# Performance work log

Hardware: AMD Instinct MI355X
Metric: run time of the kernel (lower is better)

Reference implementation:

```python
import jax, jax.numpy as jnp
import numpy as np

D_IN, D_OUT, HEADS, D_K = 256, 256, 8, 32
B, N, L = 2, 128, 512
SCALING = 1.0 / np.sqrt(D_K)


def setup_inputs() -> dict:
    key = jax.random.key(0)
    ks = jax.random.split(key, 12)
    s = 0.02
    return {
        "query": jax.random.normal(ks[0], (B, L, D_IN), jnp.float32),
        "key": jax.random.normal(ks[1], (B, L, D_IN), jnp.float32),
        "value": jax.random.normal(ks[2], (B, N, L, D_OUT), jnp.float32),
        "mask": jax.random.uniform(ks[3], (B, 1, L, L), jnp.float32),
        "Wq": jax.random.normal(ks[4], (D_IN, HEADS * D_K), jnp.float32) * s,
        "bq": jnp.zeros((HEADS * D_K,), jnp.float32),
        "Wk": jax.random.normal(ks[5], (D_IN, HEADS * D_K), jnp.float32) * s,
        "bk": jnp.zeros((HEADS * D_K,), jnp.float32),
        "Wv": jax.random.normal(ks[6], (D_OUT, D_OUT), jnp.float32) * s,
        "bv": jnp.zeros((D_OUT,), jnp.float32),
        "Wo": jax.random.normal(ks[7], (D_OUT, D_OUT), jnp.float32) * s,
        "bo": jnp.zeros((D_OUT,), jnp.float32),
    }


def reference(query, key, value, mask, Wq, bq, Wk, bk, Wv, bv, Wo, bo):
    b, n, l = value.shape[:3]
    h, dk = HEADS, D_K
    dh = value.shape[-1] // h  # per-head value dim
    # projections -> per-head layouts
    q = (query @ Wq + bq).reshape(b, l, h, dk).transpose(0, 2, 1, 3)  # bhld
    k = (key @ Wk + bk).reshape(b, l, h, dk).transpose(0, 2, 1, 3)    # bhld
    v = (value @ Wv + bv).reshape(b, n, l, h, dh).transpose(0, 3, 1, 2, 4)  # bhnld
    q = q * SCALING
    scores = jnp.einsum('bhid,bhjd->bhij', q, k)  # (B,H,L,L)
    scores = jnp.where(mask < 0.5, jnp.finfo(scores.dtype).min, scores)
    attn = jax.nn.softmax(scores, axis=-1)
    # dropout omitted (eval mode / deterministic reference)
    out = jnp.einsum('bhij,bhnjd->bhnid', attn, v)  # (B,H,N,L,dh)
    out = out.transpose(0, 2, 3, 1, 4).reshape(b, n, l, h * dh)
    return out @ Wo + bo
```

## Files before the change

### kernel.cpp

```cpp
#include <hip/hip_runtime.h>
#include <hip/hip_bf16.h>
#include <stdint.h>

#define BB 2
#define LL 512
#define DIN 256
#define HH 8
#define DKK 32
#define NN 128
#define DM 256
#define SCALING 0.17677669529663687f

typedef unsigned short u16;
typedef float f32x4 __attribute__((ext_vector_type(4)));
typedef short s16x8 __attribute__((ext_vector_type(8)));

#define MFMA16(a, b, c) __builtin_amdgcn_mfma_f32_16x16x32_bf16((a), (b), (c), 0, 0, 0)

typedef __attribute__((address_space(3))) char lds_char;
typedef const __attribute__((address_space(1))) char glb_char;

__device__ __forceinline__ void gload16(const void* g, void* l) {
    __builtin_amdgcn_global_load_lds((glb_char*)g, (lds_char*)l, 16, 0, 0);
}

__device__ __forceinline__ u16 f2bf(float f) {
    union { float f; uint32_t i; } v; v.f = f;
    uint32_t x = v.i;
    return (u16)((x + 0x7fffu + ((x >> 16) & 1u)) >> 16);
}

__device__ __forceinline__ uint32_t pack2bf(float f0, float f1) {
    union { float f; uint32_t i; } a, b;
    a.f = f0; b.f = f1;
    return __builtin_amdgcn_perm(b.i + 0x8000u, a.i + 0x8000u, 0x07060302u);
}

__device__ __forceinline__ s16x8 ldsfrag(const u16* base, int row, int cb) {
    const char* p = (const char*)base + row * 128 + (cb ^ ((row & 7) << 4));
    return *(const s16x8*)(const void*)p;
}

__global__ __launch_bounds__(256) void prep_weights(
        const float* __restrict__ Wq, const float* __restrict__ Wk,
        const float* __restrict__ Wv, const float* __restrict__ Wo,
        u16* __restrict__ wqt, u16* __restrict__ wkt,
        u16* __restrict__ wvt, u16* __restrict__ wot) {
    int idx = blockIdx.x * 256 + threadIdx.x;
    int which = idx >> 16;
    const float* src = (which == 0) ? Wq : (which == 1) ? Wk : (which == 2) ? Wv : Wo;
    u16* dst = (which == 0) ? wqt : (which == 1) ? wkt : (which == 2) ? wvt : wot;
    int i = idx & 65535;
    int c = i & 255;
    int k = i >> 8;
    dst[(size_t)c * 256 + k] = f2bf(src[(size_t)k * 256 + c]);
}

__global__ __launch_bounds__(256) void qk_proj(
        const float* __restrict__ q_in, const float* __restrict__ k_in,
        const u16* __restrict__ wqt, const float* __restrict__ bq,
        const u16* __restrict__ wkt, const float* __restrict__ bk,
        u16* __restrict__ q_ws, u16* __restrict__ k_ws) {
    int bid = blockIdx.x;
    int isK = bid & 1;
    int r0 = (bid >> 1) * 64;
    const float* src = isK ? k_in : q_in;
    const u16* wt    = isK ? wkt : wqt;
    const float* bias = isK ? bk : bq;
    u16* dst = isK ? k_ws : q_ws;
    float scale = isK ? 1.0f : SCALING;

    int t = threadIdx.x, w = t >> 6, l = t & 63, lr = l & 15, lg = l >> 4;

    f32x4 zero = {0.f, 0.f, 0.f, 0.f};
    f32x4 acc[4][4];
#pragma unroll
    for (int m = 0; m < 4; m++)
#pragma unroll
        for (int cf = 0; cf < 4; cf++) acc[m][cf] = zero;

#pragma unroll
    for (int ks = 0; ks < 8; ks++) {
        s16x8 afr[4];
#pragma unroll
        for (int m = 0; m < 4; m++) {
            const float* p = src + (size_t)(r0 + m * 16 + lr) * DIN + ks * 32 + lg * 8;
            float4 v0 = *(const float4*)p;
            float4 v1 = *(const float4*)(p + 4);
            union { u16 u[8]; s16x8 v; } tmp;
            tmp.u[0] = f2bf(v0.x); tmp.u[1] = f2bf(v0.y);
            tmp.u[2] = f2bf(v0.z); tmp.u[3] = f2bf(v0.w);
            tmp.u[4] = f2bf(v1.x); tmp.u[5] = f2bf(v1.y);
            tmp.u[6] = f2bf(v1.z); tmp.u[7] = f2bf(v1.w);
            afr[m] = tmp.v;
        }
        s16x8 bfrg[4];
#pragma unroll
        for (int cf = 0; cf < 4; cf++)
            bfrg[cf] = *(const s16x8*)(const void*)(wt + (size_t)(w * 64 + cf * 16 + lr) * 256 + ks * 32 + lg * 8);
#pragma unroll
        for (int m = 0; m < 4; m++)
#pragma unroll
            for (int cf = 0; cf < 4; cf++) acc[m][cf] = MFMA16(afr[m], bfrg[cf], acc[m][cf]);
    }

#pragma unroll
    for (int m = 0; m < 4; m++)
#pragma unroll
        for (int cf = 0; cf < 4; cf++) {
            int c = w * 64 + cf * 16 + lr;
            int h = c >> 5, dd = c & 31;
            float bv_ = bias[c];
#pragma unroll
            for (int r = 0; r < 4; r++) {
                int row = r0 + m * 16 + 4 * lg + r;
                int b = row >> 9, li = row & 511;
                dst[(((size_t)(b * HH + h)) * LL + li) * DKK + dd] = f2bf((acc[m][cf][r] + bv_) * scale);
            }
        }
}

__global__ __launch_bounds__(256) void scores_softmax(
        const u16* __restrict__ q_ws, const u16* __restrict__ k_ws,
        const float* __restrict__ mask, u16* __restrict__ attn) {
    int bid = blockIdx.x;
    int it = bid & 15;
    int bh = bid >> 4;
    int b = bh >> 3;
    int i0 = it * 32;

    __shared__ u16 kl[LL][40];
    __shared__ u16 ql[32][40];
    __shared__ float redmx[2][32];
    __shared__ float redsm[2][32];

    int t = threadIdx.x;
    const u16* kbase = k_ws + (size_t)bh * LL * DKK;
#pragma unroll
    for (int x = 0; x < 8; x++) {
        int idx = x * 256 + t;
        int row = idx >> 2, ch = idx & 3;
        *(s16x8*)(void*)(&kl[row][ch * 8]) = *(const s16x8*)(const void*)(kbase + (size_t)row * DKK + ch * 8);
    }
    if (t < 128) {
        const u16* qbase = q_ws + (size_t)bh * LL * DKK + (size_t)i0 * DKK;
        int row = t >> 2, ch = t & 3;
        *(s16x8*)(void*)(&ql[row][ch * 8]) = *(const s16x8*)(const void*)(qbase + (size_t)row * DKK + ch * 8);
    }
    __syncthreads();

    int w = t >> 6, l = t & 63, lr = l & 15, lg = l >> 4;
    int ih = (w & 1) * 16;
    int jh = (w >> 1) * 256;
    int jhalf = w >> 1;

    s16x8 af = *(const s16x8*)(const void*)(&ql[ih + lr][lg * 8]);
    f32x4 zero = {0.f, 0.f, 0.f, 0.f};
    f32x4 acc[16];
#pragma unroll
    for (int cf = 0; cf < 16; cf++) {
        s16x8 bf = *(const s16x8*)(const void*)(&kl[jh + cf * 16 + lr][lg * 8]);
        acc[cf] = MFMA16(af, bf, zero);
    }

    const float* mrow = mask + (size_t)b * LL * LL;
    float attv[16][4];
    float mx[4], sm[4];
#pragma unroll
    for (int r = 0; r < 4; r++) mx[r] = -3.0e38f;
#pragma unroll
    for (int cf = 0; cf < 16; cf++) {
#pragma unroll
        for (int r = 0; r < 4; r++) {
            int irow = i0 + ih + 4 * lg + r;
            int jcol = jh + cf * 16 + lr;
            float mv = mrow[(size_t)irow * LL + jcol];
            float s = (mv < 0.5f) ? -1.0e30f : acc[cf][r];
            attv[cf][r] = s;
            mx[r] = fmaxf(mx[r], s);
        }
    }
#pragma unroll
    for (int d = 1; d < 16; d <<= 1)
#pragma unroll
        for (int r = 0; r < 4; r++) mx[r] = fmaxf(mx[r], __shfl_xor(mx[r], d));
#pragma unroll
    for (int r = 0; r < 4; r++) sm[r] = 0.f;
#pragma unroll
    for (int cf = 0; cf < 16; cf++)
#pragma unroll
        for (int r = 0; r < 4; r++) {
            float p = __expf(attv[cf][r] - mx[r]);
            attv[cf][r] = p;
            sm[r] += p;
        }
#pragma unroll
    for (int d = 1; d < 16; d <<= 1)
#pragma unroll
        for (int r = 0; r < 4; r++) sm[r] += __shfl_xor(sm[r], d);

    if (lr == 0) {
#pragma unroll
        for (int r = 0; r < 4; r++) {
            redmx[jhalf][ih + 4 * lg + r] = mx[r];
            redsm[jhalf][ih + 4 * lg + r] = sm[r];
        }
    }
    __syncthreads();
    float inv[4];
#pragma unroll
    for (int r = 0; r < 4; r++) {
        int row = ih + 4 * lg + r;
        float m0 = redmx[0][row], m1 = redmx[1][row];
        float s0 = redsm[0][row], s1 = redsm[1][row];
        float gm = fmaxf(m0, m1);
        float gs = s0 * __expf(m0 - gm) + s1 * __expf(m1 - gm);
        inv[r] = __expf(mx[r] - gm) / gs;
    }

    u16* abase = attn + (size_t)bh * LL * LL;
#pragma unroll
    for (int cf = 0; cf < 16; cf++)
#pragma unroll
        for (int r = 0; r < 4; r++) {
            int irow = i0 + ih + 4 * lg + r;
            int jcol = jh + cf * 16 + lr;
            abase[(size_t)irow * LL + jcol] = f2bf(attv[cf][r] * inv[r]);
        }
}

__global__ __launch_bounds__(256, 2) void vproj_gemm(
        const float* __restrict__ value, const float* __restrict__ bv,
        const u16* __restrict__ wvt, u16* __restrict__ ut) {
    __shared__ __align__(16) u16 sm[2 * 16384];

    int t = threadIdx.x;
    int nb = gridDim.x;
    int cpx = nb >> 3;
    int swz = (blockIdx.x & 7) * cpx + (blockIdx.x >> 3);
    int ct = swz & 1;
    int jt = (swz >> 1) & 3;
    int bn = swz >> 3;
    int c0 = ct * 128, j0 = jt * 128;

    int w = t >> 6, l = t & 63, lr = l & 15, lg = l >> 4;
    int wr = w >> 1, wc = w & 1;

    const float* vbase = value + ((size_t)bn * LL + j0) * DM;

    int srow = t >> 3;
    int sgc = t & 7;
    f32x4 zero = {0.f, 0.f, 0.f, 0.f};
    f32x4 acc[4][4];
#pragma unroll
    for (int m = 0; m < 4; m++)
#pragma unroll
        for (int nf = 0; nf < 4; nf++) acc[m][nf] = zero;

    auto stageA = [&](int buf, int kk) {
#pragma unroll
        for (int x = 0; x < 4; x++) {
            int row = x * 32 + srow;
            int gs = sgc ^ (row & 7);
            gload16(wvt + (size_t)(c0 + row) * 256 + kk * 64 + gs * 8,
                    (char*)&sm[buf * 16384] + (x * 256 + t) * 16);
        }
    };
    float4 breg[2][4][2];
    auto loadB = [&](int set, int kk) {
#pragma unroll
        for (int x = 0; x < 4; x++) {
            int row = x * 32 + srow;
            const float* p = vbase + (size_t)row * DM + kk * 64 + sgc * 8;
            breg[set][x][0] = *(const float4*)p;
            breg[set][x][1] = *(const float4*)(p + 4);
        }
    };
    auto writeB = [&](int buf, int set) {
#pragma unroll
        for (int x = 0; x < 4; x++) {
            int row = x * 32 + srow;
            uint32_t p0 = pack2bf(breg[set][x][0].x, breg[set][x][0].y);
            uint32_t p1 = pack2bf(breg[set][x][0].z, breg[set][x][0].w);
            uint32_t p2 = pack2bf(breg[set][x][1].x, breg[set][x][1].y);
            uint32_t p3 = pack2bf(breg[set][x][1].z, breg[set][x][1].w);
            uint32_t* dst = (uint32_t*)((char*)&sm[buf * 16384 + 8192]
                            + row * 128 + ((sgc * 16) ^ ((row & 7) << 4)));
            dst[0] = p0; dst[1] = p1; dst[2] = p2; dst[3] = p3;
        }
    };

    stageA(0, 0);
    loadB(0, 0);
    loadB(1, 1);
    writeB(0, 0);
    __syncthreads();
    int cur = 0;
#pragma unroll
    for (int kk = 0; kk < 4; kk++) {
        if (kk < 3) stageA(cur ^ 1, kk + 1);
        if (kk < 2) loadB(kk & 1, kk + 2);
        const u16* Ab = &sm[cur * 16384];
        const u16* Bb = &sm[cur * 16384 + 8192];
        s16x8 af[4][2], bf[4][2];
#pragma unroll
        for (int m = 0; m < 4; m++)
#pragma unroll
            for (int ks = 0; ks < 2; ks++)
                af[m][ks] = ldsfrag(Ab, wr * 64 + m * 16 + lr, ks * 64 + lg * 16);
#pragma unroll
        for (int nf = 0; nf < 4; nf++)
#pragma unroll
            for (int ks = 0; ks < 2; ks++)
                bf[nf][ks] = ldsfrag(Bb, wc * 64 + nf * 16 + lr, ks * 64 + lg * 16);
#pragma unroll
        for (int ks = 0; ks < 2; ks++)
#pragma unroll
            for (int m = 0; m < 4; m++)
#pragma unroll
                for (int nf = 0; nf < 4; nf++)
                    acc[m][nf] = MFMA16(af[m][ks], bf[nf][ks], acc[m][nf]);
        if (kk < 3) writeB(cur ^ 1, (kk + 1) & 1);
        __syncthreads();
        cur ^= 1;
    }

    u16* ubase = ut + (size_t)bn * DM * LL;
#pragma unroll
    for (int m = 0; m < 4; m++) {
#pragma unroll
        for (int rr = 0; rr < 4; rr++) {
            int c = c0 + wr * 64 + m * 16 + 4 * lg + rr;
            float bvv = bv[c];
#pragma unroll
            for (int nf = 0; nf < 4; nf++) {
                int j = j0 + wc * 64 + nf * 16 + lr;
                ubase[(size_t)c * LL + j] = f2bf(acc[m][nf][rr] + bvv);
            }
        }
    }
}

__global__ __launch_bounds__(256, 2) void pv_gemm(
        const u16* __restrict__ attn, const u16* __restrict__ ut,
        u16* __restrict__ Tm, int n0, int nTiles, int Nc) {
    __shared__ __align__(16) u16 sm[2 * 16384];

    int t = threadIdx.x;
    int nb = gridDim.x;
    int cpx = nb >> 3;
    int swz = (blockIdx.x & 7) * cpx + (blockIdx.x >> 3);
    int nct = swz % nTiles;
    int tmp2 = swz / nTiles;
    int it = tmp2 & 3;
    int bh = tmp2 >> 2;
    int b = bh >> 3, h = bh & 7;
    int i0 = it * 128;

    int w = t >> 6, l = t & 63, lr = l & 15, lg = l >> 4;
    int wr = w >> 1, wc = w & 1;

    const u16* arow0 = attn + (size_t)bh * LL * LL + (size_t)i0 * LL;

    f32x4 zero = {0.f, 0.f, 0.f, 0.f};
    f32x4 acc[4][4];
#pragma unroll
    for (int m = 0; m < 4; m++)
#pragma unroll
        for (int nf = 0; nf < 4; nf++) acc[m][nf] = zero;

    auto stage = [&](int buf, int kk) {
#pragma unroll
        for (int x = 0; x < 4; x++) {
            int G = x * 256 + t;
            int row = G >> 3, gc = G & 7;
            int gs = gc ^ (row & 7);
            gload16(arow0 + (size_t)row * LL + kk * 64 + gs * 8,
                    (char*)&sm[buf * 16384] + G * 16);
        }
#pragma unroll
        for (int x = 0; x < 4; x++) {
            int G = x * 256 + t;
            int row = G >> 3, gc = G & 7;
            int gs = gc ^ (row & 7);
            int nc = nct * 128 + row;
            const u16* src = ut + (((size_t)(b * NN + n0 + (nc >> 5))) * DM + h * DKK + (nc & 31)) * LL
                             + kk * 64 + gs * 8;
            gload16(src, (char*)&sm[buf * 16384 + 8192] + G * 16);
        }
    };

    stage(0, 0);
    __syncthreads();
    int cur = 0;
    for (int kk = 0; kk < 8; kk++) {
        if (kk < 7) stage(cur ^ 1, kk + 1);
        const u16* Ab = &sm[cur * 16384];
        const u16* Bb = &sm[cur * 16384 + 8192];
        s16x8 af[4][2], bf[4][2];
#pragma unroll
        for (int m = 0; m < 4; m++)
#pragma unroll
            for (int ks = 0; ks < 2; ks++)
                af[m][ks] = ldsfrag(Ab, wr * 64 + m * 16 + lr, ks * 64 + lg * 16);
#pragma unroll
        for (int nf = 0; nf < 4; nf++)
#pragma unroll
            for (int ks = 0; ks < 2; ks++)
                bf[nf][ks] = ldsfrag(Bb, wc * 64 + nf * 16 + lr, ks * 64 + lg * 16);
#pragma unroll
        for (int ks = 0; ks < 2; ks++)
#pragma unroll
            for (int m = 0; m < 4; m++)
#pragma unroll
                for (int nf = 0; nf < 4; nf++)
                    acc[m][nf] = MFMA16(af[m][ks], bf[nf][ks], acc[m][nf]);
        __syncthreads();
        cur ^= 1;
    }

#pragma unroll
    for (int m = 0; m < 4; m++) {
        int i = i0 + wr * 64 + m * 16 + 4 * lg;
#pragma unroll
        for (int nf = 0; nf < 4; nf++) {
            int nc = nct * 128 + wc * 64 + nf * 16 + lr;
            int nl = nc >> 5, cl = nc & 31;
            u16* dst = Tm + (((size_t)(b * Nc + nl)) * LL + i) * DM + h * DKK + cl;
#pragma unroll
            for (int rr = 0; rr < 4; rr++)
                dst[(size_t)rr * DM] = f2bf(acc[m][nf][rr]);
        }
    }
}

__global__ __launch_bounds__(256, 2) void wo_gemm(
        const u16* __restrict__ Tm, const u16* __restrict__ wot,
        const float* __restrict__ bo, float* __restrict__ out,
        int n0, int Nc, int nshift) {
    __shared__ __align__(16) u16 sm[2 * 16384];

    int t = threadIdx.x;
    int nb = gridDim.x;
    int cpx = nb >> 3;
    int swz = (blockIdx.x & 7) * cpx + (blockIdx.x >> 3);
    int oc = swz & 1;
    int mt = swz >> 1;
    int r0 = mt * 128;

    int w = t >> 6, l = t & 63, lr = l & 15, lg = l >> 4;
    int wr = w >> 1, wc = w & 1;

    f32x4 zero = {0.f, 0.f, 0.f, 0.f};
    f32x4 acc[4][4];
#pragma unroll
    for (int m = 0; m < 4; m++)
#pragma unroll
        for (int nf = 0; nf < 4; nf++) acc[m][nf] = zero;

    auto stage = [&](int buf, int kk) {
#pragma unroll
        for (int x = 0; x < 4; x++) {
            int G = x * 256 + t;
            int row = G >> 3, gc = G & 7;
            int gs = gc ^ (row & 7);
            gload16(Tm + (size_t)(r0 + row) * DM + kk * 64 + gs * 8,
                    (char*)&sm[buf * 16384] + G * 16);
        }
#pragma unroll
        for (int x = 0; x < 4; x++) {
            int G = x * 256 + t;
            int row = G >> 3, gc = G & 7;
            int gs = gc ^ (row & 7);
            gload16(wot + (size_t)(oc * 128 + row) * DM + kk * 64 + gs * 8,
                    (char*)&sm[buf * 16384 + 8192] + G * 16);
        }
    };

    stage(0, 0);
    __syncthreads();
    int cur = 0;
    for (int kk = 0; kk < 4; kk++) {
        if (kk < 3) stage(cur ^ 1, kk + 1);
        const u16* Ab = &sm[cur * 16384];
        const u16* Bb = &sm[cur * 16384 + 8192];
        s16x8 af[4][2], bf[4][2];
#pragma unroll
        for (int m = 0; m < 4; m++)
#pragma unroll
            for (int ks = 0; ks < 2; ks++)
                af[m][ks] = ldsfrag(Ab, wr * 64 + m * 16 + lr, ks * 64 + lg * 16);
#pragma unroll
        for (int nf = 0; nf < 4; nf++)
#pragma unroll
            for (int ks = 0; ks < 2; ks++)
                bf[nf][ks] = ldsfrag(Bb, wc * 64 + nf * 16 + lr, ks * 64 + lg * 16);
#pragma unroll
        for (int ks = 0; ks < 2; ks++)
#pragma unroll
            for (int m = 0; m < 4; m++)
#pragma unroll
                for (int nf = 0; nf < 4; nf++)
                    acc[m][nf] = MFMA16(af[m][ks], bf[nf][ks], acc[m][nf]);
        __syncthreads();
        cur ^= 1;
    }

#pragma unroll
    for (int nf = 0; nf < 4; nf++) {
        int ocol = oc * 128 + wc * 64 + nf * 16 + lr;
        float bov = bo[ocol];
#pragma unroll
        for (int m = 0; m < 4; m++) {
            int rbase = r0 + wr * 64 + m * 16 + 4 * lg;
#pragma unroll
            for (int rr = 0; rr < 4; rr++) {
                int r = rbase + rr;
                int bnl = r >> 9, i = r & 511;
                int b = bnl >> nshift, nl = bnl & (Nc - 1);
                out[(((size_t)(b * NN + n0 + nl)) * LL + i) * DM + ocol] = acc[m][nf][rr] + bov;
            }
        }
    }
}

extern "C" void kernel_launch(void* const* d_in, const int* in_sizes, int n_in,
                              void* d_out, int out_size, void* d_ws, size_t ws_size,
                              hipStream_t stream) {
    const float* query = (const float*)d_in[0];
    const float* key_  = (const float*)d_in[1];
    const float* value = (const float*)d_in[2];
    const float* mask  = (const float*)d_in[3];
    const float* Wq = (const float*)d_in[4];
    const float* bq = (const float*)d_in[5];
    const float* Wk = (const float*)d_in[6];
    const float* bk = (const float*)d_in[7];
    const float* Wv = (const float*)d_in[8];
    const float* bv = (const float*)d_in[9];
    const float* Wo = (const float*)d_in[10];
    const float* bo = (const float*)d_in[11];

    char* ws = (char*)d_ws;
    u16* wvt  = (u16*)(ws + 0);
    u16* wot  = (u16*)(ws + 131072);
    u16* qw   = (u16*)(ws + 262144);
    u16* kw   = (u16*)(ws + 786432);
    u16* attn = (u16*)(ws + 1310720);
    u16* wqt  = (u16*)(ws + 1310720);
    u16* wkt  = (u16*)(ws + 1310720 + 131072);
    u16* ut   = (u16*)(ws + 9699328);
    u16* Tm   = (u16*)(ws + 76808192);
    float* out = (float*)d_out;

    size_t avail = (ws_size > 76808192u) ? (ws_size - 76808192u) : 0;
    int Nc = 128;
    while (Nc > 4 && (size_t)Nc * 524288u > avail) Nc >>= 1;
    int nshift = 0;
    while ((1 << nshift) < Nc) nshift++;

    hipLaunchKernelGGL(prep_weights,   dim3(1024), dim3(256), 0, stream, Wq, Wk, Wv, Wo, wqt, wkt, wvt, wot);
    hipLaunchKernelGGL(qk_proj,        dim3(32),   dim3(256), 0, stream, query, key_, wqt, bq, wkt, bk, qw, kw);
    hipLaunchKernelGGL(scores_softmax, dim3(256),  dim3(256), 0, stream, qw, kw, mask, attn);
    hipLaunchKernelGGL(vproj_gemm,     dim3(2048), dim3(256), 0, stream, value, bv, wvt, ut);

    int nTiles = Nc >> 2;
    for (int n0 = 0; n0 < NN; n0 += Nc) {
        hipLaunchKernelGGL(pv_gemm, dim3(16 * 4 * nTiles), dim3(256), 0, stream,
                           attn, ut, Tm, n0, nTiles, Nc);
        hipLaunchKernelGGL(wo_gemm, dim3((BB * Nc * LL / 128) * 2), dim3(256), 0, stream,
                           Tm, wot, bo, out, n0, Nc, nshift);
    }
}
```

Before: 185.0 us.

## Deepen pv_gemm pipeline to four stages with BK=32 and vmcnt waits

Reworks the PV GEMM main loop from a double-buffered BK=64 pipeline into a four-buffer BK=32 ring with three stages of loads in flight. It uses explicit s_waitcnt vmcnt counts and a single barrier per iteration instead of waiting on all loads and syncing twice. The goal is to hide global-to-LDS load latency behind MFMA work. LDS size stays the same, but there are twice as many iterations and barriers, and the swizzle for the 64-byte rows now only spreads over 4 positions, which may cause more bank conflicts.

```diff
diff --git a/kernel.cpp b/kernel.cpp
--- a/kernel.cpp
+++ b/kernel.cpp
@@ -38,6 +38,11 @@
 
 __device__ __forceinline__ s16x8 ldsfrag(const u16* base, int row, int cb) {
     const char* p = (const char*)base + row * 128 + (cb ^ ((row & 7) << 4));
+    return *(const s16x8*)(const void*)p;
+}
+
+__device__ __forceinline__ s16x8 ldsfrag32(const u16* base, int row, int lg) {
+    const char* p = (const char*)base + row * 64 + ((lg * 16) ^ ((row & 3) << 4));
     return *(const s16x8*)(const void*)p;
 }
 
@@ -344,7 +349,7 @@
 __global__ __launch_bounds__(256, 2) void pv_gemm(
         const u16* __restrict__ attn, const u16* __restrict__ ut,
         u16* __restrict__ Tm, int n0, int nTiles, int Nc) {
-    __shared__ __align__(16) u16 sm[2 * 16384];
+    __shared__ __align__(16) u16 sm[4 * 8192];
 
     int t = threadIdx.x;
     int nb = gridDim.x;
@@ -371,52 +376,49 @@
 
     auto stage = [&](int buf, int kk) {
 #pragma unroll
-        for (int x = 0; x < 4; x++) {
+        for (int x = 0; x < 2; x++) {
             int G = x * 256 + t;
-            int row = G >> 3, gc = G & 7;
-            int gs = gc ^ (row & 7);
-            gload16(arow0 + (size_t)row * LL + kk * 64 + gs * 8,
-                    (char*)&sm[buf * 16384] + G * 16);
-        }
-#pragma unroll
-        for (int x = 0; x < 4; x++) {
+            int row = G >> 2, gc = G & 3;
+            int gs = gc ^ (row & 3);
+            gload16(arow0 + (size_t)row * LL + kk * 32 + gs * 8,
+                    (char*)&sm[buf * 8192] + G * 16);
+        }
+#pragma unroll
+        for (int x = 0; x < 2; x++) {
             int G = x * 256 + t;
-            int row = G >> 3, gc = G & 7;
-            int gs = gc ^ (row & 7);
+            int row = G >> 2, gc = G & 3;
+            int gs = gc ^ (row & 3);
             int nc = nct * 128 + row;
             const u16* src = ut + (((size_t)(b * NN + n0 + (nc >> 5))) * DM + h * DKK + (nc & 31)) * LL
-                             + kk * 64 + gs * 8;
-            gload16(src, (char*)&sm[buf * 16384 + 8192] + G * 16);
+                             + kk * 32 + gs * 8;
+            gload16(src, (char*)&sm[buf * 8192 + 4096] + G * 16);
         }
     };
 
     stage(0, 0);
-    __syncthreads();
-    int cur = 0;
-    for (int kk = 0; kk < 8; kk++) {
-        if (kk < 7) stage(cur ^ 1, kk + 1);
-        const u16* Ab = &sm[cur * 16384];
-        const u16* Bb = &sm[cur * 16384 + 8192];
-        s16x8 af[4][2], bf[4][2];
+    stage(1, 1);
+    stage(2, 2);
+#pragma unroll
+    for (int kk = 0; kk < 16; kk++) {
+        if (kk <= 13)      asm volatile("s_waitcnt vmcnt(8)" ::: "memory");
+        else if (kk == 14) asm volatile("s_waitcnt vmcnt(4)" ::: "memory");
+        else               asm volatile("s_waitcnt vmcnt(0)" ::: "memory");
+        __builtin_amdgcn_s_barrier();
+        if (kk < 13) stage((kk + 3) & 3, kk + 3);
+        const u16* Ab = &sm[(kk & 3) * 8192];
+        const u16* Bb = &sm[(kk & 3) * 8192 + 4096];
+        s16x8 af[4], bf[4];
 #pragma unroll
         for (int m = 0; m < 4; m++)
-#pragma unroll
-            for (int ks = 0; ks < 2; ks++)
-                af[m][ks] = ldsfrag(Ab, wr * 64 + m * 16 + lr, ks * 64 + lg * 16);
+            af[m] = ldsfrag32(Ab, wr * 64 + m * 16 + lr, lg);
 #pragma unroll
         for (int nf = 0; nf < 4; nf++)
-#pragma unroll
-            for (int ks = 0; ks < 2; ks++)
-                bf[nf][ks] = ldsfrag(Bb, wc * 64 + nf * 16 + lr, ks * 64 + lg * 16);
-#pragma unroll
-        for (int ks = 0; ks < 2; ks++)
-#pragma unroll
-            for (int m = 0; m < 4; m++)
-#pragma unroll
-                for (int nf = 0; nf < 4; nf++)
-                    acc[m][nf] = MFMA16(af[m][ks], bf[nf][ks], acc[m][nf]);
-        __syncthreads();
-        cur ^= 1;
+            bf[nf] = ldsfrag32(Bb, wc * 64 + nf * 16 + lr, lg);
+#pragma unroll
+        for (int m = 0; m < 4; m++)
+#pragma unroll
+            for (int nf = 0; nf < 4; nf++)
+                acc[m][nf] = MFMA16(af[m], bf[nf], acc[m][nf]);
     }
 
 #pragma unroll
```

Result: slower. 192.6 us (+4.1%).

## Fuse scores-softmax and V projection into one heterogeneous launch

Applied to the files above, without the earlier changes.

Merges the independent scores/softmax kernel and the V-projection GEMM into a single grid, where block index selects which task to run. This removes one launch and lets the small softmax work overlap with the large GEMM instead of running serially. The fused kernel loses the explicit launch bounds and the softmax blocks now reserve the larger shared buffer, which may change register allocation and occupancy.

```diff
diff --git a/kernel.cpp b/kernel.cpp
--- a/kernel.cpp
+++ b/kernel.cpp
@@ -120,224 +120,223 @@
         }
 }
 
-__global__ __launch_bounds__(256) void scores_softmax(
+__global__ void sv_fused(
+        const float* __restrict__ value, const float* __restrict__ bv,
+        const u16* __restrict__ wvt, u16* __restrict__ ut,
         const u16* __restrict__ q_ws, const u16* __restrict__ k_ws,
         const float* __restrict__ mask, u16* __restrict__ attn) {
-    int bid = blockIdx.x;
-    int it = bid & 15;
-    int bh = bid >> 4;
-    int b = bh >> 3;
-    int i0 = it * 32;
-
-    __shared__ u16 kl[LL][40];
-    __shared__ u16 ql[32][40];
-    __shared__ float redmx[2][32];
-    __shared__ float redsm[2][32];
+    __shared__ __align__(16) u16 sm[2 * 16384];
 
     int t = threadIdx.x;
-    const u16* kbase = k_ws + (size_t)bh * LL * DKK;
-#pragma unroll
-    for (int x = 0; x < 8; x++) {
-        int idx = x * 256 + t;
-        int row = idx >> 2, ch = idx & 3;
-        *(s16x8*)(void*)(&kl[row][ch * 8]) = *(const s16x8*)(const void*)(kbase + (size_t)row * DKK + ch * 8);
-    }
-    if (t < 128) {
-        const u16* qbase = q_ws + (size_t)bh * LL * DKK + (size_t)i0 * DKK;
-        int row = t >> 2, ch = t & 3;
-        *(s16x8*)(void*)(&ql[row][ch * 8]) = *(const s16x8*)(const void*)(qbase + (size_t)row * DKK + ch * 8);
-    }
-    __syncthreads();
-
     int w = t >> 6, l = t & 63, lr = l & 15, lg = l >> 4;
-    int ih = (w & 1) * 16;
-    int jh = (w >> 1) * 256;
-    int jhalf = w >> 1;
-
-    s16x8 af = *(const s16x8*)(const void*)(&ql[ih + lr][lg * 8]);
-    f32x4 zero = {0.f, 0.f, 0.f, 0.f};
-    f32x4 acc[16];
-#pragma unroll
-    for (int cf = 0; cf < 16; cf++) {
-        s16x8 bf = *(const s16x8*)(const void*)(&kl[jh + cf * 16 + lr][lg * 8]);
-        acc[cf] = MFMA16(af, bf, zero);
-    }
-
-    const float* mrow = mask + (size_t)b * LL * LL;
-    float attv[16][4];
-    float mx[4], sm[4];
-#pragma unroll
-    for (int r = 0; r < 4; r++) mx[r] = -3.0e38f;
-#pragma unroll
-    for (int cf = 0; cf < 16; cf++) {
+
+    if (blockIdx.x < 2048) {
+        int bid = blockIdx.x;
+        int cpx = 2048 >> 3;
+        int swz = (bid & 7) * cpx + (bid >> 3);
+        int ct = swz & 1;
+        int jt = (swz >> 1) & 3;
+        int bn = swz >> 3;
+        int c0 = ct * 128, j0 = jt * 128;
+        int wr = w >> 1, wc = w & 1;
+
+        const float* vbase = value + ((size_t)bn * LL + j0) * DM;
+        int srow = t >> 3;
+        int sgc = t & 7;
+        f32x4 zero = {0.f, 0.f, 0.f, 0.f};
+        f32x4 acc[4][4];
+#pragma unroll
+        for (int m = 0; m < 4; m++)
+#pragma unroll
+            for (int nf = 0; nf < 4; nf++) acc[m][nf] = zero;
+
+        auto stageA = [&](int buf, int kk) {
+#pragma unroll
+            for (int x = 0; x < 4; x++) {
+                int row = x * 32 + srow;
+                int gs = sgc ^ (row & 7);
+                gload16(wvt + (size_t)(c0 + row) * 256 + kk * 64 + gs * 8,
+                        (char*)&sm[buf * 16384] + (x * 256 + t) * 16);
+            }
+        };
+        float4 breg[2][4][2];
+        auto loadB = [&](int set, int kk) {
+#pragma unroll
+            for (int x = 0; x < 4; x++) {
+                int row = x * 32 + srow;
+                const float* p = vbase + (size_t)row * DM + kk * 64 + sgc * 8;
+                breg[set][x][0] = *(const float4*)p;
+                breg[set][x][1] = *(const float4*)(p + 4);
+            }
+        };
+        auto writeB = [&](int buf, int set) {
+#pragma unroll
+            for (int x = 0; x < 4; x++) {
+                int row = x * 32 + srow;
+                uint32_t p0 = pack2bf(breg[set][x][0].x, breg[set][x][0].y);
+                uint32_t p1 = pack2bf(breg[set][x][0].z, breg[set][x][0].w);
+                uint32_t p2 = pack2bf(breg[set][x][1].x, breg[set][x][1].y);
+                uint32_t p3 = pack2bf(breg[set][x][1].z, breg[set][x][1].w);
+                uint32_t* dst = (uint32_t*)((char*)&sm[buf * 16384 + 8192]
+                                + row * 128 + ((sgc * 16) ^ ((row & 7) << 4)));
+                dst[0] = p0; dst[1] = p1; dst[2] = p2; dst[3] = p3;
+            }
+        };
+
+        stageA(0, 0);
+        loadB(0, 0);
+        loadB(1, 1);
+        writeB(0, 0);
+        __syncthreads();
+        int cur = 0;
+#pragma unroll
+        for (int kk = 0; kk < 4; kk++) {
+            if (kk < 3) stageA(cur ^ 1, kk + 1);
+            if (kk < 2) loadB(kk & 1, kk + 2);
+            const u16* Ab = &sm[cur * 16384];
+            const u16* Bb = &sm[cur * 16384 + 8192];
+            s16x8 af[4][2], bf[4][2];
+#pragma unroll
+            for (int m = 0; m < 4; m++)
+#pragma unroll
+                for (int ks = 0; ks < 2; ks++)
+                    af[m][ks] = ldsfrag(Ab, wr * 64 + m * 16 + lr, ks * 64 + lg * 16);
+#pragma unroll
+            for (int nf = 0; nf < 4; nf++)
+#pragma unroll
+                for (int ks = 0; ks < 2; ks++)
+                    bf[nf][ks] = ldsfrag(Bb, wc * 64 + nf * 16 + lr, ks * 64 + lg * 16);
+#pragma unroll
+            for (int ks = 0; ks < 2; ks++)
+#pragma unroll
+                for (int m = 0; m < 4; m++)
+#pragma unroll
+                    for (int nf = 0; nf < 4; nf++)
+                        acc[m][nf] = MFMA16(af[m][ks], bf[nf][ks], acc[m][nf]);
+            if (kk < 3) writeB(cur ^ 1, (kk + 1) & 1);
+            __syncthreads();
+            cur ^= 1;
+        }
+
+        u16* ubase = ut + (size_t)bn * DM * LL;
+#pragma unroll
+        for (int m = 0; m < 4; m++) {
+#pragma unroll
+            for (int rr = 0; rr < 4; rr++) {
+                int c = c0 + wr * 64 + m * 16 + 4 * lg + rr;
+                float bvv = bv[c];
+#pragma unroll
+                for (int nf = 0; nf < 4; nf++) {
+                    int j = j0 + wc * 64 + nf * 16 + lr;
+                    ubase[(size_t)c * LL + j] = f2bf(acc[m][nf][rr] + bvv);
+                }
+            }
+        }
+    } else {
+        int bid = blockIdx.x - 2048;
+        int it = bid & 15;
+        int bh = bid >> 4;
+        int b = bh >> 3;
+        int i0 = it * 32;
+
+        u16* kl_ = sm;
+        u16* ql_ = sm + 20480;
+        float* redmx_ = (float*)(void*)(sm + 21760);
+        float* redsm_ = redmx_ + 64;
+
+        const u16* kbase = k_ws + (size_t)bh * LL * DKK;
+#pragma unroll
+        for (int x = 0; x < 8; x++) {
+            int idx = x * 256 + t;
+            int row = idx >> 2, ch = idx & 3;
+            *(s16x8*)(void*)(kl_ + row * 40 + ch * 8) =
+                *(const s16x8*)(const void*)(kbase + (size_t)row * DKK + ch * 8);
+        }
+        if (t < 128) {
+            const u16* qbase = q_ws + (size_t)bh * LL * DKK + (size_t)i0 * DKK;
+            int row = t >> 2, ch = t & 3;
+            *(s16x8*)(void*)(ql_ + row * 40 + ch * 8) =
+                *(const s16x8*)(const void*)(qbase + (size_t)row * DKK + ch * 8);
+        }
+        __syncthreads();
+
+        int ih = (w & 1) * 16;
+        int jh = (w >> 1) * 256;
+        int jhalf = w >> 1;
+
+        s16x8 af = *(const s16x8*)(const void*)(ql_ + (ih + lr) * 40 + lg * 8);
+        f32x4 zero = {0.f, 0.f, 0.f, 0.f};
+        f32x4 acc[16];
+#pragma unroll
+        for (int cf = 0; cf < 16; cf++) {
+            s16x8 bf = *(const s16x8*)(const void*)(kl_ + (jh + cf * 16 + lr) * 40 + lg * 8);
+            acc[cf] = MFMA16(af, bf, zero);
+        }
+
+        const float* mrow = mask + (size_t)b * LL * LL;
+        float attv[16][4];
+        float mx[4], smax[4];
+#pragma unroll
+        for (int r = 0; r < 4; r++) mx[r] = -3.0e38f;
+#pragma unroll
+        for (int cf = 0; cf < 16; cf++) {
+#pragma unroll
+            for (int r = 0; r < 4; r++) {
+                int irow = i0 + ih + 4 * lg + r;
+                int jcol = jh + cf * 16 + lr;
+                float mv = mrow[(size_t)irow * LL + jcol];
+                float s = (mv < 0.5f) ? -1.0e30f : acc[cf][r];
+                attv[cf][r] = s;
+                mx[r] = fmaxf(mx[r], s);
+            }
+        }
+#pragma unroll
+        for (int d = 1; d < 16; d <<= 1)
+#pragma unroll
+            for (int r = 0; r < 4; r++) mx[r] = fmaxf(mx[r], __shfl_xor(mx[r], d));
+#pragma unroll
+        for (int r = 0; r < 4; r++) smax[r] = 0.f;
+#pragma unroll
+        for (int cf = 0; cf < 16; cf++)
+#pragma unroll
+            for (int r = 0; r < 4; r++) {
+                float p = __expf(attv[cf][r] - mx[r]);
+                attv[cf][r] = p;
+                smax[r] += p;
+            }
+#pragma unroll
+        for (int d = 1; d < 16; d <<= 1)
+#pragma unroll
+            for (int r = 0; r < 4; r++) smax[r] += __shfl_xor(smax[r], d);
+
+        if (lr == 0) {
+#pragma unroll
+            for (int r = 0; r < 4; r++) {
+                redmx_[jhalf * 32 + ih + 4 * lg + r] = mx[r];
+                redsm_[jhalf * 32 + ih + 4 * lg + r] = smax[r];
+            }
+        }
+        __syncthreads();
+        float inv[4];
 #pragma unroll
         for (int r = 0; r < 4; r++) {
-            int irow = i0 + ih + 4 * lg + r;
-            int jcol = jh + cf * 16 + lr;
-            float mv = mrow[(size_t)irow * LL + jcol];
-            float s = (mv < 0.5f) ? -1.0e30f : acc[cf][r];
-            attv[cf][r] = s;
-            mx[r] = fmaxf(mx[r], s);
-        }
-    }
-#pragma unroll
-    for (int d = 1; d < 16; d <<= 1)
-#pragma unroll
-        for (int r = 0; r < 4; r++) mx[r] = fmaxf(mx[r], __shfl_xor(mx[r], d));
-#pragma unroll
-    for (int r = 0; r < 4; r++) sm[r] = 0.f;
-#pragma unroll
-    for (int cf = 0; cf < 16; cf++)
-#pragma unroll
-        for (int r = 0; r < 4; r++) {
-            float p = __expf(attv[cf][r] - mx[r]);
-            attv[cf][r] = p;
-            sm[r] += p;
-        }
-#pragma unroll
-    for (int d = 1; d < 16; d <<= 1)
-#pragma unroll
-        for (int r = 0; r < 4; r++) sm[r] += __shfl_xor(sm[r], d);
-
-    if (lr == 0) {
-#pragma unroll
-        for (int r = 0; r < 4; r++) {
-            redmx[jhalf][ih + 4 * lg + r] = mx[r];
-            redsm[jhalf][ih + 4 * lg + r] = sm[r];
-        }
-    }
-    __syncthreads();
-    float inv[4];
-#pragma unroll
-    for (int r = 0; r < 4; r++) {
-        int row = ih + 4 * lg + r;
-        float m0 = redmx[0][row], m1 = redmx[1][row];
-        float s0 = redsm[0][row], s1 = redsm[1][row];
-        float gm = fmaxf(m0, m1);
-        float gs = s0 * __expf(m0 - gm) + s1 * __expf(m1 - gm);
-        inv[r] = __expf(mx[r] - gm) / gs;
-    }
-
-    u16* abase = attn + (size_t)bh * LL * LL;
-#pragma unroll
-    for (int cf = 0; cf < 16; cf++)
-#pragma unroll
-        for (int r = 0; r < 4; r++) {
-            int irow = i0 + ih + 4 * lg + r;
-            int jcol = jh + cf * 16 + lr;
-            abase[(size_t)irow * LL + jcol] = f2bf(attv[cf][r] * inv[r]);
-        }
-}
-
-__global__ __launch_bounds__(256, 2) void vproj_gemm(
-        const float* __restrict__ value, const float* __restrict__ bv,
-        const u16* __restrict__ wvt, u16* __restrict__ ut) {
-    __shared__ __align__(16) u16 sm[2 * 16384];
-
-    int t = threadIdx.x;
-    int nb = gridDim.x;
-    int cpx = nb >> 3;
-    int swz = (blockIdx.x & 7) * cpx + (blockIdx.x >> 3);
-    int ct = swz & 1;
-    int jt = (swz >> 1) & 3;
-    int bn = swz >> 3;
-    int c0 = ct * 128, j0 = jt * 128;
-
-    int w = t >> 6, l = t & 63, lr = l & 15, lg = l >> 4;
-    int wr = w >> 1, wc = w & 1;
-
-    const float* vbase = value + ((size_t)bn * LL + j0) * DM;
-
-    int srow = t >> 3;
-    int sgc = t & 7;
-    f32x4 zero = {0.f, 0.f, 0.f, 0.f};
-    f32x4 acc[4][4];
-#pragma unroll
-    for (int m = 0; m < 4; m++)
-#pragma unroll
-        for (int nf = 0; nf < 4; nf++) acc[m][nf] = zero;
-
-    auto stageA = [&](int buf, int kk) {
-#pragma unroll
-        for (int x = 0; x < 4; x++) {
-            int row = x * 32 + srow;
-            int gs = sgc ^ (row & 7);
-            gload16(wvt + (size_t)(c0 + row) * 256 + kk * 64 + gs * 8,
-                    (char*)&sm[buf * 16384] + (x * 256 + t) * 16);
-        }
-    };
-    float4 breg[2][4][2];
-    auto loadB = [&](int set, int kk) {
-#pragma unroll
-        for (int x = 0; x < 4; x++) {
-            int row = x * 32 + srow;
-            const float* p = vbase + (size_t)row * DM + kk * 64 + sgc * 8;
-            breg[set][x][0] = *(const float4*)p;
-            breg[set][x][1] = *(const float4*)(p + 4);
-        }
-    };
-    auto writeB = [&](int buf, int set) {
-#pragma unroll
-        for (int x = 0; x < 4; x++) {
-            int row = x * 32 + srow;
-            uint32_t p0 = pack2bf(breg[set][x][0].x, breg[set][x][0].y);
-            uint32_t p1 = pack2bf(breg[set][x][0].z, breg[set][x][0].w);
-            uint32_t p2 = pack2bf(breg[set][x][1].x, breg[set][x][1].y);
-            uint32_t p3 = pack2bf(breg[set][x][1].z, breg[set][x][1].w);
-            uint32_t* dst = (uint32_t*)((char*)&sm[buf * 16384 + 8192]
-                            + row * 128 + ((sgc * 16) ^ ((row & 7) << 4)));
-            dst[0] = p0; dst[1] = p1; dst[2] = p2; dst[3] = p3;
-        }
-    };
-
-    stageA(0, 0);
-    loadB(0, 0);
-    loadB(1, 1);
-    writeB(0, 0);
-    __syncthreads();
-    int cur = 0;
-#pragma unroll
-    for (int kk = 0; kk < 4; kk++) {
-        if (kk < 3) stageA(cur ^ 1, kk + 1);
-        if (kk < 2) loadB(kk & 1, kk + 2);
-        const u16* Ab = &sm[cur * 16384];
-        const u16* Bb = &sm[cur * 16384 + 8192];
-        s16x8 af[4][2], bf[4][2];
-#pragma unroll
-        for (int m = 0; m < 4; m++)
-#pragma unroll
-            for (int ks = 0; ks < 2; ks++)
-                af[m][ks] = ldsfrag(Ab, wr * 64 + m * 16 + lr, ks * 64 + lg * 16);
-#pragma unroll
-        for (int nf = 0; nf < 4; nf++)
-#pragma unroll
-            for (int ks = 0; ks < 2; ks++)
-                bf[nf][ks] = ldsfrag(Bb, wc * 64 + nf * 16 + lr, ks * 64 + lg * 16);
-#pragma unroll
-        for (int ks = 0; ks < 2; ks++)
-#pragma unroll
-            for (int m = 0; m < 4; m++)
-#pragma unroll
-                for (int nf = 0; nf < 4; nf++)
-                    acc[m][nf] = MFMA16(af[m][ks], bf[nf][ks], acc[m][nf]);
-        if (kk < 3) writeB(cur ^ 1, (kk + 1) & 1);
-        __syncthreads();
-        cur ^= 1;
-    }
-
-    u16* ubase = ut + (size_t)bn * DM * LL;
-#pragma unroll
-    for (int m = 0; m < 4; m++) {
-#pragma unroll
-        for (int rr = 0; rr < 4; rr++) {
-            int c = c0 + wr * 64 + m * 16 + 4 * lg + rr;
-            float bvv = bv[c];
-#pragma unroll
-            for (int nf = 0; nf < 4; nf++) {
-                int j = j0 + wc * 64 + nf * 16 + lr;
-                ubase[(size_t)c * LL + j] = f2bf(acc[m][nf][rr] + bvv);
-            }
-        }
+            int row = ih + 4 * lg + r;
+            float m0 = redmx_[row], m1 = redmx_[32 + row];
+            float s0 = redsm_[row], s1 = redsm_[32 + row];
+            float gm = fmaxf(m0, m1);
+            float gs = s0 * __expf(m0 - gm) + s1 * __expf(m1 - gm);
+            inv[r] = __expf(mx[r] - gm) / gs;
+        }
+
+        u16* abase = attn + (size_t)bh * LL * LL;
+#pragma unroll
+        for (int cf = 0; cf < 16; cf++)
+#pragma unroll
+            for (int r = 0; r < 4; r++) {
+                int irow = i0 + ih + 4 * lg + r;
+                int jcol = jh + cf * 16 + lr;
+                abase[(size_t)irow * LL + jcol] = f2bf(attv[cf][r] * inv[r]);
+            }
     }
 }
 
@@ -558,10 +557,10 @@
     int nshift = 0;
     while ((1 << nshift) < Nc) nshift++;
 
-    hipLaunchKernelGGL(prep_weights,   dim3(1024), dim3(256), 0, stream, Wq, Wk, Wv, Wo, wqt, wkt, wvt, wot);
-    hipLaunchKernelGGL(qk_proj,        dim3(32),   dim3(256), 0, stream, query, key_, wqt, bq, wkt, bk, qw, kw);
-    hipLaunchKernelGGL(scores_softmax, dim3(256),  dim3(256), 0, stream, qw, kw, mask, attn);
-    hipLaunchKernelGGL(vproj_gemm,     dim3(2048), dim3(256), 0, stream, value, bv, wvt, ut);
+    hipLaunchKernelGGL(prep_weights, dim3(1024), dim3(256), 0, stream, Wq, Wk, Wv, Wo, wqt, wkt, wvt, wot);
+    hipLaunchKernelGGL(qk_proj,      dim3(32),   dim3(256), 0, stream, query, key_, wqt, bq, wkt, bk, qw, kw);
+    hipLaunchKernelGGL(sv_fused,     dim3(2304), dim3(256), 0, stream,
+                       value, bv, wvt, ut, qw, kw, mask, attn);
 
     int nTiles = Nc >> 2;
     for (int n0 = 0; n0 < NN; n0 += Nc) {
```

Measured after the change: 232.1 us. 25.4% more time.
